# Optimization experiments

Hardware: AMD Instinct MI355X
Metric: run time of the kernel (lower is better)

## Reference

```python
import jax, jax.numpy as jnp
import numpy as np

NUM_CLASSES = 80
IGNORE_THRESH = 0.7
COORD_SCALE = 1.0
NOOBJ_SCALE = 1.0
OBJ_SCALE = 5.0
CLASS_SCALE = 1.0
NUM_A = 3  # anchors per scale


def iou_cxcywh(a, b):
    """Elementwise/broadcast IoU for boxes in (cx, cy, w, h) format."""
    tl = jnp.maximum(a[..., :2] - a[..., 2:] * 0.5, b[..., :2] - b[..., 2:] * 0.5)
    br = jnp.minimum(a[..., :2] + a[..., 2:] * 0.5, b[..., :2] + b[..., 2:] * 0.5)
    wh = jnp.clip(br - tl, 0.0)
    inter = wh[..., 0] * wh[..., 1]
    union = a[..., 2] * a[..., 3] + b[..., 2] * b[..., 3] - inter
    return inter / union


def yolo_scale_loss(out, targets, anchors):
    B, C, H, W = out.shape
    A, nc = NUM_A, NUM_CLASSES
    HW = H * W
    # ---------------- target building (on detached outputs) ----------------
    od = jax.lax.stop_gradient(out).reshape(B, A, 5 + nc, H, W).transpose(0, 1, 3, 4, 2)  # B,A,H,W,85
    xs = jnp.arange(W, dtype=out.dtype)
    ys = jnp.arange(H, dtype=out.dtype)
    px = jax.nn.sigmoid(od[..., 0]) + xs[None, None, None, :]
    py = jax.nn.sigmoid(od[..., 1]) + ys[None, None, :, None]
    pw = jnp.exp(od[..., 2]) * anchors[:, 0][None, :, None, None]
    ph = jnp.exp(od[..., 3]) * anchors[:, 1][None, :, None, None]
    pred = jnp.stack([px, py, pw, ph], -1).transpose(0, 2, 3, 1, 4)  # B,H,W,A,4
    pred = pred.reshape(B, HW, A, 4)

    Y, X = jnp.meshgrid(jnp.arange(H, dtype=out.dtype), jnp.arange(W, dtype=out.dtype), indexing='ij')
    cell = jnp.stack([X, Y], -1).reshape(HW, 1, 2)  # cell corner (x1y1)
    anc_x1y1 = jnp.concatenate([jnp.broadcast_to(cell, (HW, A, 2)),
                                jnp.broadcast_to(anchors[None], (HW, A, 2))], -1)  # HW,A,4
    anc_xcyc = anc_x1y1.at[..., :2].add(0.5)

    valid = targets.sum(axis=2) > 0  # [B,K] padded-front object mask
    num_obj = valid.sum(axis=1)
    K = targets.shape[1]
    gt = targets[..., :4] * jnp.array([W, H, W, H], dtype=out.dtype)  # grid units
    gt_cls = targets[..., 4].astype(jnp.int32)

    # IoU of every prediction vs every gt: [B, HW*A, K]
    ious = iou_cxcywh(pred.reshape(B, HW * A, 1, 4), gt[:, None, :, :])
    ious = jnp.where(valid[:, None, :], ious, -1.0)
    max_iou = ious.max(-1).reshape(B, HW, A)

    has_pos = (max_iou > IGNORE_THRESH).reshape(B, -1).any(axis=1)
    iou_mask = jnp.full((B, HW, A), NOOBJ_SCALE, dtype=out.dtype)
    iou_mask = jnp.where(has_pos[:, None, None] & (max_iou >= IGNORE_THRESH), 0.0, iou_mask)
    iou_mask = jnp.where((num_obj > 0)[:, None, None], iou_mask, 0.0)

    # per-object responsible cell + anchor
    cx = jnp.clip(jnp.floor(gt[..., 0]), 0, W - 1).astype(jnp.int32)  # [B,K]
    cy = jnp.clip(jnp.floor(gt[..., 1]), 0, H - 1).astype(jnp.int32)
    cell_idx = cy * W + cx
    a_boxes = anc_xcyc[cell_idx]  # [B,K,A,4]
    ov = iou_cxcywh(a_boxes, gt[:, :, None, :])  # [B,K,A]
    a_star = jnp.argmax(ov, -1).astype(jnp.int32)  # [B,K]

    resp = anc_x1y1[cell_idx, a_star]  # [B,K,4] responsible anchor (x1,y1,w,h)
    delta = jnp.stack([gt[..., 0] - resp[..., 0], gt[..., 1] - resp[..., 1],
                       gt[..., 2] / resp[..., 2], gt[..., 3] / resp[..., 3]], -1)  # [B,K,4]
    bidx = jnp.arange(B, dtype=jnp.int32)[:, None]
    obj_iou = max_iou[bidx, cell_idx, a_star]  # [B,K]

    N = B * HW * A
    f = (jnp.arange(B, dtype=jnp.int32)[:, None] * (HW * A) + cell_idx * A + a_star)  # [B,K]
    rank = jnp.arange(B * K, dtype=jnp.int32).reshape(B, K)
    rank_m = jnp.where(valid, rank, -1)
    seg = jax.ops.segment_max(rank_m.ravel(), f.ravel(), num_segments=N)
    winner = valid & (rank == seg[f])
    f_eff = jnp.where(winner, f, N).ravel()  # losers -> dummy slot

    box_target = jnp.zeros((N + 1, 4), out.dtype).at[f_eff].set(delta.reshape(-1, 4))[:-1]
    box_mask = jnp.zeros(N + 1, out.dtype).at[f_eff].set(1.0)[:-1]
    class_target = jnp.zeros(N + 1, jnp.int32).at[f_eff].set(gt_cls.ravel())[:-1]
    class_mask = box_mask
    iou_target = jnp.zeros(N + 1, out.dtype).at[f_eff].set(obj_iou.ravel())[:-1]
    iou_mask = jnp.concatenate([iou_mask.ravel(), jnp.zeros(1, out.dtype)]).at[f_eff].set(OBJ_SCALE)[:-1]

    # ---------------- loss on live outputs ----------------
    o = out.reshape(B, A, 5 + nc, H, W).transpose(0, 3, 4, 1, 2).reshape(N, 5 + nc)
    pred_delta = jnp.concatenate([jax.nn.sigmoid(o[:, :2]), jnp.exp(o[:, 2:4])], axis=1)
    pred_conf = jax.nn.sigmoid(o[:, 4])
    logits = o[:, 5:]

    box_loss = jnp.sum(box_mask[:, None] * (pred_delta - box_target) ** 2)
    iou_loss = jnp.sum((pred_conf * iou_mask - iou_target * iou_mask) ** 2)
    lse = jax.nn.logsumexp(logits, axis=-1)
    tgt_logit = jnp.take_along_axis(logits, class_target[:, None], axis=1)[:, 0]
    class_loss = jnp.sum(class_mask * (lse - tgt_logit))

    return (box_loss * COORD_SCALE / 2.0 + iou_loss / 2.0 + class_loss * CLASS_SCALE) / B


def reference(o1, o2, o3, targets, anchors):
    # anchor_mask = [[6,7,8],[3,4,5],[0,1,2]]
    l1 = yolo_scale_loss(o1, targets, anchors[6:9])
    l2 = yolo_scale_loss(o2, targets, anchors[3:6])
    l3 = yolo_scale_loss(o3, targets, anchors[0:3])
    return (l1 + l2 + l3) / 3.0


def setup_inputs() -> dict:
    key = jax.random.key(0)
    ks = jax.random.split(key, 5)
    B, K, nc = 16, 50, 80
    o1 = jax.random.normal(ks[0], (B, 255, 13, 13), jnp.float32)
    o2 = jax.random.normal(ks[1], (B, 255, 26, 26), jnp.float32)
    o3 = jax.random.normal(ks[2], (B, 255, 52, 52), jnp.float32)
    boxes = jax.random.uniform(ks[3], (B, K, 4), jnp.float32, 0.05, 0.95)
    cls = jax.random.randint(ks[4], (B, K, 1), 0, nc).astype(jnp.float32)
    targets = jnp.concatenate([boxes, cls], axis=-1)
    anchors_px = np.array([[10, 13], [16, 30], [33, 23], [30, 61], [62, 45],
                           [59, 119], [116, 90], [156, 198], [373, 326]], np.float32)
    strides = np.array([8, 8, 8, 16, 16, 16, 32, 32, 32], np.float32)[:, None]
    anchors = jnp.asarray(anchors_px / strides)
    return {"o1": o1, "o2": o2, "o3": o3, "targets": targets, "anchors": anchors}
```

## Files before the change

kernel.cpp:

```cpp
#include <hip/hip_runtime.h>

static constexpr int Bn = 16, Kn = 50, NCn = 80;
static constexpr int NTOT = 16 * 3 * (169 + 676 + 2704);
static constexpr int NBLK_A = (NTOT + 255) / 256;
static constexpr int NBLK_ASSIGN = 12;
static constexpr int NREC = 3 * Bn * Kn;
static constexpr int NBLK_F = NREC / 4;
static constexpr int MIOU_OFF = 0;
static constexpr int NO_OFF   = 170352;
static constexpr int REC_OFF  = 170368;
static constexpr int EXPC_OFF = 189568;
static constexpr int EXPD_OFF = 190240;
static constexpr int PARTF_OFF = 200896;
static constexpr float IGN = 0.7f;
static constexpr float W_BOX = 1.0f / 96.0f;
static constexpr float W_IOU = 1.0f / 96.0f;
static constexpr float W_CLS = 1.0f / 48.0f;

__device__ __forceinline__ float sigf(float x) { return 1.0f / (1.0f + __expf(-x)); }

__device__ __forceinline__ float iou_box(float ax, float ay, float aw, float ah,
                                         float bx, float by, float bw, float bh) {
  float tlx = fmaxf(ax - aw * 0.5f, bx - bw * 0.5f);
  float tly = fmaxf(ay - ah * 0.5f, by - bh * 0.5f);
  float brx = fminf(ax + aw * 0.5f, bx + bw * 0.5f);
  float bry = fminf(ay + ah * 0.5f, by + bh * 0.5f);
  float w = fmaxf(brx - tlx, 0.0f);
  float h = fmaxf(bry - tly, 0.0f);
  float inter = w * h;
  float uni = aw * ah + bw * bh - inter;
  return inter / uni;
}

__device__ __forceinline__ void decode_cell(int g, int& s, int& H, int& HW,
                                            int& base, int& b, int& a, int& hw) {
  if (g < 8112)       { s = 0; H = 13; HW = 169;  base = 0; }
  else if (g < 40560) { s = 1; H = 26; HW = 676;  base = 8112; }
  else                { s = 2; H = 52; HW = 2704; base = 40560; }
  int local = g - base;
  hw = local % HW;
  int t = local / HW;
  a = t % 3;
  b = t / 3;
}

__global__ __launch_bounds__(256) void kMain(const float* __restrict__ o0,
                                             const float* __restrict__ o1,
                                             const float* __restrict__ o2,
                                             const float* __restrict__ tgt,
                                             const float* __restrict__ anc,
                                             float* __restrict__ ws) {
  __shared__ float tg[Bn * Kn * 5];
  __shared__ float ls1[48], ls2[48], lhp[48];
  __shared__ int lcnt;
  int tid = threadIdx.x;
  for (int i = tid; i < Bn * Kn * 5; i += 256) tg[i] = tgt[i];
  if (tid < 48) { ls1[tid] = 0.0f; ls2[tid] = 0.0f; lhp[tid] = 0.0f; }
  if (tid == 0) lcnt = 0;
  __syncthreads();

  if (blockIdx.x >= NBLK_A) {
    int wv = (blockIdx.x - NBLK_A) * 4 + (tid >> 6);
    int lane = tid & 63;
    int s = wv / 16, b = wv % 16;
    int H, HW, base;
    if (s == 0)      { H = 13; HW = 169;  base = 0; }
    else if (s == 1) { H = 26; HW = 676;  base = 8112; }
    else             { H = 52; HW = 2704; base = 40560; }
    int W = H;
    int aoff = 6 - 3 * s;
    float aw0 = anc[aoff * 2],       ah0 = anc[aoff * 2 + 1];
    float aw1 = anc[(aoff + 1) * 2], ah1 = anc[(aoff + 1) * 2 + 1];
    float aw2 = anc[(aoff + 2) * 2], ah2 = anc[(aoff + 2) * 2 + 1];

    bool valid = false;
    int gslot = -1 - lane;
    float dx = 0, dy = 0, dw = 0, dh = 0, tc = 0;
    if (lane < Kn) {
      const float* tp = &tg[(b * Kn + lane) * 5];
      float tx = tp[0], ty = tp[1], tw = tp[2], th = tp[3];
      tc = tp[4];
      if (tx + ty + tw + th + tc > 0.0f) {
        valid = true;
        float gx = tx * W, gy = ty * H, gw = tw * W, gh = th * H;
        int cx = (int)floorf(gx); cx = min(max(cx, 0), W - 1);
        int cy = (int)floorf(gy); cy = min(max(cy, 0), H - 1);
        float ccx = cx + 0.5f, ccy = cy + 0.5f;
        float i0 = iou_box(ccx, ccy, aw0, ah0, gx, gy, gw, gh);
        float i1 = iou_box(ccx, ccy, aw1, ah1, gx, gy, gw, gh);
        float i2 = iou_box(ccx, ccy, aw2, ah2, gx, gy, gw, gh);
        int astar = 0; float bi = i0;
        if (i1 > bi) { bi = i1; astar = 1; }
        if (i2 > bi) { bi = i2; astar = 2; }
        float raw = (astar == 0) ? aw0 : (astar == 1) ? aw1 : aw2;
        float rah = (astar == 0) ? ah0 : (astar == 1) ? ah1 : ah2;
        gslot = base + (b * 3 + astar) * HW + cy * W + cx;
        dx = gx - (float)cx;
        dy = gy - (float)cy;
        dw = gw / raw;
        dh = gh / rah;
      }
    }
    bool win = valid;
    for (int k2 = 1; k2 < Kn; k2++) {
      int other = __shfl(gslot, k2);
      if (k2 > lane && other == gslot) win = false;
    }
    unsigned long long bal = __ballot(valid);
    if (lane == 0 && s == 0) ((int*)ws)[NO_OFF + b] = (int)__popcll(bal);
    if (lane < Kn) {
      float* r = ws + REC_OFF + (size_t)(wv * Kn + lane) * 8;
      r[0] = win ? 1.0f : 0.0f;
      r[1] = __int_as_float(gslot);
      r[2] = dx; r[3] = dy; r[4] = dw; r[5] = dh;
      r[6] = tc;
      r[7] = 0.0f;
    }
    return;
  }

  int g = blockIdx.x * 256 + tid;
  if (g < NTOT) {
    int s, H, HW, base, b, a, hw;
    decode_cell(g, s, H, HW, base, b, a, hw);
    int W = H;
    const float* o = (s == 0) ? o0 : (s == 1) ? o1 : o2;
    int x = hw % W, y = hw / W;
    int aoff = 6 - 3 * s;
    float aw = anc[(aoff + a) * 2], ah = anc[(aoff + a) * 2 + 1];
    int ob = (b * 255 + a * 85) * HW + hw;
    float px = sigf(o[ob]) + (float)x;
    float py = sigf(o[ob + HW]) + (float)y;
    float pw = __expf(o[ob + 2 * HW]) * aw;
    float ph = __expf(o[ob + 3 * HW]) * ah;
    float conf = sigf(o[ob + 4 * HW]);
    float pxl = px - pw * 0.5f, pxr = px + pw * 0.5f;
    float pyl = py - ph * 0.5f, pyr = py + ph * 0.5f;
    float parea = pw * ph;
    float bi = -1.0f, bu = 1.0f;
    const float* tb = &tg[b * Kn * 5];
    for (int k = 0; k < Kn; k++) {
      float gx = tb[k * 5], gy = tb[k * 5 + 1], gw = tb[k * 5 + 2];
      float gh = tb[k * 5 + 3], gc = tb[k * 5 + 4];
      if (gx + gy + gw + gh + gc > 0.0f) {
        float bx = gx * W, by = gy * H, bw = gw * W, bh = gh * H;
        float tlx = fmaxf(pxl, bx - bw * 0.5f);
        float tly = fmaxf(pyl, by - bh * 0.5f);
        float brx = fminf(pxr, bx + bw * 0.5f);
        float bry = fminf(pyr, by + bh * 0.5f);
        float w = fmaxf(brx - tlx, 0.0f);
        float h = fmaxf(bry - tly, 0.0f);
        float inter = w * h;
        float uni = parea + bw * bh - inter;
        if (inter * bu > bi * uni) { bi = inter; bu = uni; }
      }
    }
    float mi = bi / bu;
    ws[MIOU_OFF + g] = mi;
    int key = s * 16 + b;
    float c2 = conf * conf;
    atomicAdd(&ls1[key], c2);
    if (mi >= IGN) atomicAdd(&ls2[key], c2);
    if (mi > IGN) lhp[key] = 1.0f;
  }
  __syncthreads();
  if (tid < 48 && ls1[tid] != 0.0f) {
    int p = atomicAdd(&lcnt, 1);
    float* e = ws + EXPD_OFF + (size_t)blockIdx.x * 16 + p * 4;
    e[0] = __int_as_float(tid);
    e[1] = ls1[tid];
    e[2] = ls2[tid];
    e[3] = lhp[tid];
  }
  __syncthreads();
  if (tid == 0) ((int*)ws)[EXPC_OFF + blockIdx.x] = lcnt;
}

__global__ __launch_bounds__(256) void kFinal(const float* __restrict__ o0,
                                              const float* __restrict__ o1,
                                              const float* __restrict__ o2,
                                              float* __restrict__ ws) {
  __shared__ float wsum[4];
  int tid = threadIdx.x;
  int lane = tid & 63;
  int idx = (blockIdx.x * 256 + tid) >> 6;
  float contrib = 0.0f;

  const float* r = ws + REC_OFF + (size_t)idx * 8;
  if (r[0] != 0.0f) {
    int g = __float_as_int(r[1]);
    int s, H, HW, base, b, a, hw;
    decode_cell(g, s, H, HW, base, b, a, hw);
    const float* o = (s == 0) ? o0 : (s == 1) ? o1 : o2;
    int ob = (b * 255 + a * 85) * HW + hw;
    float l1 = (lane < NCn) ? o[ob + (5 + lane) * HW] : -1e30f;
    float l2 = (lane + 64 < NCn) ? o[ob + (5 + lane + 64) * HW] : -1e30f;
    float mx = fmaxf(l1, l2);
    for (int off = 32; off > 0; off >>= 1) mx = fmaxf(mx, __shfl_xor(mx, off));
    float sm = __expf(l1 - mx) + __expf(l2 - mx);
    for (int off = 32; off > 0; off >>= 1) sm += __shfl_xor(sm, off);
    if (lane == 0) {
      float lse = mx + __logf(sm);
      int cls = (int)r[6];
      float tgtl = o[ob + (5 + cls) * HW];
      float d0 = sigf(o[ob]) - r[2];
      float d1 = sigf(o[ob + HW]) - r[3];
      float d2 = __expf(o[ob + 2 * HW]) - r[4];
      float d3 = __expf(o[ob + 3 * HW]) - r[5];
      float box = d0 * d0 + d1 * d1 + d2 * d2 + d3 * d3;
      float conf = sigf(o[ob + 4 * HW]);
      float mi = ws[MIOU_OFF + g];
      float basem = (mi >= IGN) ? 0.0f : 1.0f;
      float vb = conf * basem;
      float dv = 5.0f * (conf - mi);
      float iouc = dv * dv - vb * vb;
      contrib += box * W_BOX + iouc * W_IOU + (lse - tgtl) * W_CLS;
    }
  }

  for (int off = 32; off > 0; off >>= 1) contrib += __shfl_down(contrib, off);
  if (lane == 0) wsum[tid >> 6] = contrib;
  __syncthreads();
  if (tid == 0)
    ws[PARTF_OFF + blockIdx.x] = wsum[0] + wsum[1] + wsum[2] + wsum[3];
}

__global__ __launch_bounds__(256) void kSum(const float* __restrict__ ws,
                                            float* __restrict__ out) {
  __shared__ float S1L[48], S2L[48], HPL[48];
  __shared__ float bsum[4];
  int tid = threadIdx.x;
  if (tid < 48) { S1L[tid] = 0.0f; S2L[tid] = 0.0f; HPL[tid] = 0.0f; }
  __syncthreads();
  for (int bid = tid; bid < NBLK_A; bid += 256) {
    int cnt = ((const int*)ws)[EXPC_OFF + bid];
    const float* e = ws + EXPD_OFF + (size_t)bid * 16;
    for (int j = 0; j < cnt; j++) {
      int key = __float_as_int(e[j * 4]);
      atomicAdd(&S1L[key], e[j * 4 + 1]);
      atomicAdd(&S2L[key], e[j * 4 + 2]);
      if (e[j * 4 + 3] != 0.0f) HPL[key] = 1.0f;
    }
  }
  __syncthreads();
  float c = 0.0f;
  if (tid < 48) {
    int b = tid & 15;
    int nobj = ((const int*)ws)[NO_OFF + b];
    if (nobj > 0)
      c += ((HPL[tid] > 0.0f) ? (S1L[tid] - S2L[tid]) : S1L[tid]) * W_IOU;
  }
  for (int i = tid; i < NBLK_F; i += 256) c += ws[PARTF_OFF + i];
  for (int off = 32; off > 0; off >>= 1) c += __shfl_down(c, off);
  if ((tid & 63) == 0) bsum[tid >> 6] = c;
  __syncthreads();
  if (tid == 0) out[0] = bsum[0] + bsum[1] + bsum[2] + bsum[3];
}

extern "C" void kernel_launch(void* const* d_in, const int* in_sizes, int n_in,
                              void* d_out, int out_size, void* d_ws, size_t ws_size,
                              hipStream_t stream) {
  const float* o0  = (const float*)d_in[0];
  const float* o1  = (const float*)d_in[1];
  const float* o2  = (const float*)d_in[2];
  const float* tgt = (const float*)d_in[3];
  const float* anc = (const float*)d_in[4];
  float* ws  = (float*)d_ws;
  float* out = (float*)d_out;

  kMain<<<NBLK_A + NBLK_ASSIGN, 256, 0, stream>>>(o0, o1, o2, tgt, anc, ws);
  kFinal<<<NBLK_F, 256, 0, stream>>>(o0, o1, o2, ws);
  kSum<<<1, 256, 0, stream>>>(ws, out);
}
```

Before: 116.6 us.

## Precompute GT corner boxes in shared memory and fuse final sum via last-block ticket

Main IoU blocks now precompute each target's normalized corners as float4 plus an area/validity float in shared memory, which removes the per-iteration validity sum, scaling and half-width math from the 50-target inner loop. The target copy is now done only by the assignment blocks. The separate single-block kSum launch is removed: kFinal blocks atomically accumulate their partials and the last block, chosen by a ticket counter, performs the final reduction. This saves a kernel launch, but the float atomics make summation order nondeterministic and the code relies on kMain resetting the counter.

```diff
diff --git a/kernel.cpp b/kernel.cpp
--- a/kernel.cpp
+++ b/kernel.cpp
@@ -11,7 +11,8 @@
 static constexpr int REC_OFF  = 170368;
 static constexpr int EXPC_OFF = 189568;
 static constexpr int EXPD_OFF = 190240;
-static constexpr int PARTF_OFF = 200896;
+static constexpr int CNT_OFF  = 200896;
+static constexpr int ACC_OFF  = 200897;
 static constexpr float IGN = 0.7f;
 static constexpr float W_BOX = 1.0f / 96.0f;
 static constexpr float W_IOU = 1.0f / 96.0f;
@@ -51,15 +52,19 @@
                                              const float* __restrict__ anc,
                                              float* __restrict__ ws) {
   __shared__ float tg[Bn * Kn * 5];
+  __shared__ float4 tga[Bn * Kn];
+  __shared__ float  tgb[Bn * Kn];
   __shared__ float ls1[48], ls2[48], lhp[48];
   __shared__ int lcnt;
   int tid = threadIdx.x;
-  for (int i = tid; i < Bn * Kn * 5; i += 256) tg[i] = tgt[i];
-  if (tid < 48) { ls1[tid] = 0.0f; ls2[tid] = 0.0f; lhp[tid] = 0.0f; }
-  if (tid == 0) lcnt = 0;
-  __syncthreads();
 
   if (blockIdx.x >= NBLK_A) {
+    for (int i = tid; i < Bn * Kn * 5; i += 256) tg[i] = tgt[i];
+    if (blockIdx.x == NBLK_A && tid == 0) {
+      ((int*)ws)[CNT_OFF] = 0;
+      ws[ACC_OFF] = 0.0f;
+    }
+    __syncthreads();
     int wv = (blockIdx.x - NBLK_A) * 4 + (tid >> 6);
     int lane = tid & 63;
     int s = wv / 16, b = wv % 16;
@@ -119,11 +124,23 @@
     return;
   }
 
+  for (int i = tid; i < Bn * Kn; i += 256) {
+    const float* tp = tgt + (size_t)i * 5;
+    float tx = tp[0], ty = tp[1], tw = tp[2], th = tp[3], tc = tp[4];
+    float hw_ = tw * 0.5f, hh_ = th * 0.5f;
+    tga[i] = make_float4(tx - hw_, ty - hh_, tx + hw_, ty + hh_);
+    tgb[i] = (tx + ty + tw + th + tc > 0.0f) ? tw * th : -1.0f;
+  }
+  if (tid < 48) { ls1[tid] = 0.0f; ls2[tid] = 0.0f; lhp[tid] = 0.0f; }
+  if (tid == 0) lcnt = 0;
+  __syncthreads();
+
   int g = blockIdx.x * 256 + tid;
   if (g < NTOT) {
     int s, H, HW, base, b, a, hw;
     decode_cell(g, s, H, HW, base, b, a, hw);
     int W = H;
+    float Wf = (float)W, W2 = Wf * Wf;
     const float* o = (s == 0) ? o0 : (s == 1) ? o1 : o2;
     int x = hw % W, y = hw / W;
     int aoff = 6 - 3 * s;
@@ -138,20 +155,20 @@
     float pyl = py - ph * 0.5f, pyr = py + ph * 0.5f;
     float parea = pw * ph;
     float bi = -1.0f, bu = 1.0f;
-    const float* tb = &tg[b * Kn * 5];
+    const float4* ca = &tga[b * Kn];
+    const float*  cb = &tgb[b * Kn];
     for (int k = 0; k < Kn; k++) {
-      float gx = tb[k * 5], gy = tb[k * 5 + 1], gw = tb[k * 5 + 2];
-      float gh = tb[k * 5 + 3], gc = tb[k * 5 + 4];
-      if (gx + gy + gw + gh + gc > 0.0f) {
-        float bx = gx * W, by = gy * H, bw = gw * W, bh = gh * H;
-        float tlx = fmaxf(pxl, bx - bw * 0.5f);
-        float tly = fmaxf(pyl, by - bh * 0.5f);
-        float brx = fminf(pxr, bx + bw * 0.5f);
-        float bry = fminf(pyr, by + bh * 0.5f);
+      float fa = cb[k];
+      if (fa >= 0.0f) {
+        float4 c = ca[k];
+        float tlx = fmaxf(pxl, c.x * Wf);
+        float tly = fmaxf(pyl, c.y * Wf);
+        float brx = fminf(pxr, c.z * Wf);
+        float bry = fminf(pyr, c.w * Wf);
         float w = fmaxf(brx - tlx, 0.0f);
         float h = fmaxf(bry - tly, 0.0f);
         float inter = w * h;
-        float uni = parea + bw * bh - inter;
+        float uni = parea + fa * W2 - inter;
         if (inter * bu > bi * uni) { bi = inter; bu = uni; }
       }
     }
@@ -179,8 +196,11 @@
 __global__ __launch_bounds__(256) void kFinal(const float* __restrict__ o0,
                                               const float* __restrict__ o1,
                                               const float* __restrict__ o2,
-                                              float* __restrict__ ws) {
+                                              float* __restrict__ ws,
+                                              float* __restrict__ out) {
   __shared__ float wsum[4];
+  __shared__ int amLast;
+  __shared__ float S1L[48], S2L[48], HPL[48];
   int tid = threadIdx.x;
   int lane = tid & 63;
   int idx = (blockIdx.x * 256 + tid) >> 6;
@@ -221,15 +241,17 @@
   for (int off = 32; off > 0; off >>= 1) contrib += __shfl_down(contrib, off);
   if (lane == 0) wsum[tid >> 6] = contrib;
   __syncthreads();
-  if (tid == 0)
-    ws[PARTF_OFF + blockIdx.x] = wsum[0] + wsum[1] + wsum[2] + wsum[3];
-}
-
-__global__ __launch_bounds__(256) void kSum(const float* __restrict__ ws,
-                                            float* __restrict__ out) {
-  __shared__ float S1L[48], S2L[48], HPL[48];
-  __shared__ float bsum[4];
-  int tid = threadIdx.x;
+  if (tid == 0) {
+    float t = wsum[0] + wsum[1] + wsum[2] + wsum[3];
+    if (t != 0.0f) atomicAdd(&ws[ACC_OFF], t);
+    __threadfence();
+    int ticket = atomicAdd((int*)ws + CNT_OFF, 1);
+    amLast = (ticket == NBLK_F - 1);
+  }
+  __syncthreads();
+  if (!amLast) return;
+
+  __threadfence();
   if (tid < 48) { S1L[tid] = 0.0f; S2L[tid] = 0.0f; HPL[tid] = 0.0f; }
   __syncthreads();
   for (int bid = tid; bid < NBLK_A; bid += 256) {
@@ -250,11 +272,14 @@
     if (nobj > 0)
       c += ((HPL[tid] > 0.0f) ? (S1L[tid] - S2L[tid]) : S1L[tid]) * W_IOU;
   }
-  for (int i = tid; i < NBLK_F; i += 256) c += ws[PARTF_OFF + i];
   for (int off = 32; off > 0; off >>= 1) c += __shfl_down(c, off);
-  if ((tid & 63) == 0) bsum[tid >> 6] = c;
-  __syncthreads();
-  if (tid == 0) out[0] = bsum[0] + bsum[1] + bsum[2] + bsum[3];
+  if (lane == 0) wsum[tid >> 6] = c;
+  __syncthreads();
+  if (tid == 0) {
+    float fix = wsum[0] + wsum[1] + wsum[2] + wsum[3];
+    float acc = atomicAdd(&ws[ACC_OFF], 0.0f);
+    out[0] = acc + fix;
+  }
 }
 
 extern "C" void kernel_launch(void* const* d_in, const int* in_sizes, int n_in,
@@ -269,6 +294,5 @@
   float* out = (float*)d_out;
 
   kMain<<<NBLK_A + NBLK_ASSIGN, 256, 0, stream>>>(o0, o1, o2, tgt, anc, ws);
-  kFinal<<<NBLK_F, 256, 0, stream>>>(o0, o1, o2, ws);
-  kSum<<<1, 256, 0, stream>>>(ws, out);
-}
+  kFinal<<<NBLK_F, 256, 0, stream>>>(o0, o1, o2, ws, out);
+}
```

New measurement: 127.2 us. +9.0%, slower.
